# Optimization experiments

Measured on AMD Instinct MI355X. Metric: run time of the kernel, lower is better.

## Reference

```python
import jax, jax.numpy as jnp
import numpy as np

N = 50000     # nodes
E = 800000    # edges (avg degree 16)
IN = 128
HID = 128
OUT = 128


def _init_lin(key, n_out, n_in, bias=True):
    k1, k2 = jax.random.split(key)
    bound = 1.0 / np.sqrt(n_in)
    W = jax.random.uniform(k1, (n_out, n_in), minval=-bound, maxval=bound, dtype=jnp.float32)
    if bias:
        b = jax.random.uniform(k2, (n_out,), minval=-bound, maxval=bound, dtype=jnp.float32)
        return W, b
    return W


def setup_inputs() -> dict:
    key = jax.random.key(0)
    ks = jax.random.split(key, 20)
    inp = {
        "s": jax.random.normal(ks[0], (N, IN), dtype=jnp.float32),
        "t": jax.random.normal(ks[1], (N, IN), dtype=jnp.float32),
        "edge_index": jax.random.randint(ks[2], (2, E), 0, N, dtype=jnp.int64),
        "edge_weight": jax.random.normal(ks[3], (E,), dtype=jnp.float32),
    }
    dims = [(HID, IN), (OUT, HID)]
    i = 4
    for layer in range(2):
        n_out, n_in = dims[layer]
        for pre in ("s", "t"):
            Wl, bl = _init_lin(ks[i], n_out, n_in, bias=True); i += 1
            Wr = _init_lin(ks[i], n_out, n_in, bias=False); i += 1
            inp[f"{pre}{layer}_Wl"] = Wl
            inp[f"{pre}{layer}_bl"] = bl
            inp[f"{pre}{layer}_Wr"] = Wr
    return inp


def _sage(x, src, dst, w, Wl, bl, Wr):
    """SAGEConv (mean aggr, weighted messages): lin_l(mean_j w_ij x_j) + lin_r(x_i)."""
    n = x.shape[0]
    msg = x[src] * w[:, None]                                   # [E, d] gather
    agg = jax.ops.segment_sum(msg, dst, num_segments=n)         # [N, d] scatter-add
    cnt = jax.ops.segment_sum(jnp.ones_like(w), dst, num_segments=n)
    mean = agg / jnp.maximum(cnt, 1.0)[:, None]
    return mean @ Wl.T + bl + x @ Wr.T


def reference(s, t, edge_index, edge_weight,
              s0_Wl, s0_bl, s0_Wr, t0_Wl, t0_bl, t0_Wr,
              s1_Wl, s1_bl, s1_Wr, t1_Wl, t1_bl, t1_Wr):
    w = jax.nn.sigmoid(edge_weight)
    src, dst = edge_index[0], edge_index[1]
    # layer 0 (relu; dropout is identity in eval mode)
    s1 = jax.nn.relu(_sage(t, src, dst, w, s0_Wl, s0_bl, s0_Wr))
    t1 = jax.nn.relu(_sage(s, dst, src, w, t0_Wl, t0_bl, t0_Wr))  # flipped edges
    # layer 1 (no activation)
    s2 = _sage(t1, src, dst, w, s1_Wl, s1_bl, s1_Wr)
    t2 = _sage(s1, dst, src, w, t1_Wl, t1_bl, t1_Wr)
    return (s2, t2)
```

## Files before the change

kernel.cpp:

```cpp
#include <hip/hip_runtime.h>
#include <hip/hip_bf16.h>

#define DIM 128
#define BINSHIFT 8
#define BINSZ 256
#define MAXBINS2 400
#define EPB 2048
#define CAP 6144

typedef __attribute__((ext_vector_type(4))) float f32x4;
typedef __attribute__((ext_vector_type(8))) _Float16 h16x8;
typedef __attribute__((ext_vector_type(2))) _Float16 h16x2;
typedef __attribute__((ext_vector_type(8))) unsigned short u16x8;

static __device__ __forceinline__ unsigned short f2h(float f) {
    _Float16 h = (_Float16)f;
    return __builtin_bit_cast(unsigned short, h);
}

#if __has_builtin(__builtin_amdgcn_fdot2)
static __device__ __forceinline__ float dot2(h16x2 a, h16x2 b, float c) {
    return __builtin_amdgcn_fdot2(a, b, c, false);
}
#else
static __device__ __forceinline__ float dot2(h16x2 a, h16x2 b, float c) {
    return c + (float)a.x * (float)b.x + (float)a.y * (float)b.y;
}
#endif

struct WPtrs { const float* Wl[4]; const float* Wr[4]; };

__global__ __launch_bounds__(256) void dgnn_prep(
        const float* __restrict__ s, const float* __restrict__ t,
        unsigned short* __restrict__ sb, unsigned short* __restrict__ tb,
        int n4, int cvtb, WPtrs wp, unsigned short* __restrict__ Wc, int wbase,
        int* __restrict__ binCur, int nb2) {
    int b = blockIdx.x;
    if (b < wbase) {
        int which = (b >= cvtb) ? 1 : 0;
        int i = (b - which * cvtb) * 256 + threadIdx.x;
        if (i >= n4) return;
        const float* src = which ? t : s;
        unsigned short* dst = which ? tb : sb;
        float4 v = ((const float4*)src)[i];
        ushort4 o;
        o.x = f2h(v.x); o.y = f2h(v.y); o.z = f2h(v.z); o.w = f2h(v.w);
        ((ushort4*)dst)[i] = o;
    } else if (b < wbase + 128) {
        int tid = (b - wbase) * 256 + threadIdx.x;
        int i4 = tid << 2;
        int conv = i4 >> 15;
        int rem = i4 & 32767;
        int ch = rem >> 8;
        int k = rem & 255;
        const float* src = (k < 128) ? wp.Wl[conv] : wp.Wr[conv];
        float4 v = *(const float4*)(src + ch * DIM + (k & 127));
        ushort4 o;
        o.x = f2h(v.x); o.y = f2h(v.y); o.z = f2h(v.z); o.w = f2h(v.w);
        *(ushort4*)(Wc + i4) = o;
    } else {
        for (int i = threadIdx.x; i < nb2; i += 256) binCur[i] = 0;
    }
}

__global__ __launch_bounds__(256) void dgnn_binscatter(const float* __restrict__ ew,
        const int* __restrict__ srcI, const int* __restrict__ dstI,
        int* __restrict__ binCur, int2* __restrict__ binned, int E, int NBINS) {
    __shared__ int hist[MAXBINS2];
    __shared__ int epk[EPB];
    __shared__ int ewb[EPB];
    const int nb2 = 2 * NBINS;
    for (int i = threadIdx.x; i < nb2; i += 256) hist[i] = 0;
    __syncthreads();
    int base = blockIdx.x * EPB;
    int end = min(base + EPB, E);
    int cnt = end - base;
    for (int j = threadIdx.x; j < cnt; j += 256) {
        int e = base + j;
        int d = dstI[e], s = srcI[e];
        float x = ew[e];
        float w = 1.0f / (1.0f + expf(-x));
        epk[j] = d | (s << 16);
        ewb[j] = __float_as_int(w);
        atomicAdd(&hist[d >> BINSHIFT], 1);
        atomicAdd(&hist[NBINS + (s >> BINSHIFT)], 1);
    }
    __syncthreads();
    for (int i = threadIdx.x; i < nb2; i += 256) {
        int c = hist[i];
        int st = c ? atomicAdd(&binCur[i], c) : 0;
        hist[i] = i * CAP + st;
    }
    __syncthreads();
    for (int j = threadIdx.x; j < cnt; j += 256) {
        int pk = epk[j];
        int wb = ewb[j];
        int d = pk & 0xffff, s = (pk >> 16) & 0xffff;
        int pd = atomicAdd(&hist[d >> BINSHIFT], 1);
        binned[pd] = make_int2(pk, wb);
        int ps = atomicAdd(&hist[NBINS + (s >> BINSHIFT)], 1);
        binned[ps] = make_int2(pk, wb);
    }
}

__global__ __launch_bounds__(256) void dgnn_csrfinal(const int2* __restrict__ binned,
        const int* __restrict__ binCur,
        int* __restrict__ offsD, int* __restrict__ degD,
        int* __restrict__ offsS, int* __restrict__ degS,
        unsigned int* __restrict__ nbrPD, unsigned int* __restrict__ nbrPS,
        int N, int NBINS) {
    int b = blockIdx.x;
    bool isD = b < NBINS;
    int lb = isD ? b : b - NBINS;
    int nodeBase = lb << BINSHIFT;
    const int2* bin = binned + (size_t)b * CAP;
    int K = binCur[b]; if (K > CAP) K = CAP;
    int* offs = isD ? offsD : offsS;
    int* dga  = isD ? degD : degS;
    unsigned int* out = (isD ? nbrPD : nbrPS) + (size_t)lb * CAP;

    __shared__ int cnt[BINSZ], cur[BINSZ], scanb[BINSZ];
    cnt[threadIdx.x] = 0;
    __syncthreads();
    for (int i = threadIdx.x; i < K; i += 256) {
        int pk = bin[i].x;
        int node = isD ? (pk & 0xffff) : ((pk >> 16) & 0xffff);
        atomicAdd(&cnt[node - nodeBase], 1);
    }
    __syncthreads();
    int v = cnt[threadIdx.x];
    scanb[threadIdx.x] = v;
    __syncthreads();
#pragma unroll
    for (int o = 1; o < 256; o <<= 1) {
        int u = (threadIdx.x >= o) ? scanb[threadIdx.x - o] : 0;
        __syncthreads();
        scanb[threadIdx.x] += u;
        __syncthreads();
    }
    int pos = scanb[threadIdx.x] - v;
    cur[threadIdx.x] = pos;
    int n = nodeBase + threadIdx.x;
    if (n < N) { offs[n] = lb * CAP + pos; dga[n] = v; }
    __syncthreads();
    for (int i = threadIdx.x; i < K; i += 256) {
        int2 en = bin[i];
        int node, nbr;
        if (isD) { node = en.x & 0xffff; nbr = (en.x >> 16) & 0xffff; }
        else     { node = (en.x >> 16) & 0xffff; nbr = en.x & 0xffff; }
        int p = atomicAdd(&cur[node - nodeBase], 1);
        unsigned short wh = f2h(__int_as_float(en.y));
        out[p] = (unsigned int)nbr | ((unsigned int)wh << 16);
    }
}

__global__ __launch_bounds__(256, 8) void dgnn_gather2(
        const unsigned short* __restrict__ xbD, const int* __restrict__ offsD,
        const int* __restrict__ degD, const unsigned int* __restrict__ nbrD,
        unsigned short* __restrict__ meanD,
        const unsigned short* __restrict__ xbS, const int* __restrict__ offsS,
        const int* __restrict__ degS, const unsigned int* __restrict__ nbrS,
        unsigned short* __restrict__ meanS,
        int N, int halfb) {
    int which = (blockIdx.x >= halfb) ? 1 : 0;
    const unsigned short* xb = which ? xbS : xbD;
    const int* offs          = which ? offsS : offsD;
    const int* dga           = which ? degS : degD;
    const unsigned int* nbrP = which ? nbrS : nbrD;
    unsigned short* meanb    = which ? meanS : meanD;

    long long gid = (long long)(blockIdx.x - which * halfb) * 256 + threadIdx.x;
    int n = (int)(gid >> 5);
    if (n >= N) return;
    const int l32 = (int)gid & 31;
    const int q2  = l32 >> 4;
    const int m   = l32 & 15;

    int beg = offs[n];
    int dg  = dga[n];
    int end = beg + dg;
    float acc[8];
#pragma unroll
    for (int k = 0; k < 8; k++) acc[k] = 0.f;

    for (int base = beg; base < end; base += 32) {
        int cnt = end - base; if (cnt > 32) cnt = 32;
        bool inb = (base + l32) < end;
        unsigned int pk_l = inb ? nbrP[base + l32] : 0u;

        int it = 0;
        for (; it + 16 <= cnt; it += 16) {
            int e0 = it + (q2 << 1);
            unsigned int p[8];
#pragma unroll
            for (int j = 0; j < 4; j++) {
                p[2 * j]     = __shfl(pk_l, e0 + 4 * j, 32);
                p[2 * j + 1] = __shfl(pk_l, e0 + 4 * j + 1, 32);
            }
            uint4 v[8];
#pragma unroll
            for (int j = 0; j < 8; j++)
                v[j] = *(const uint4*)(xb + ((size_t)(p[j] & 0xffffu) << 7) + (m << 3));
#pragma unroll
            for (int j = 0; j < 4; j++) {
                h16x2 wp = __builtin_bit_cast(h16x2,
                    __builtin_amdgcn_perm(p[2 * j + 1], p[2 * j], 0x07060302u));
                const unsigned int* ua = &v[2 * j].x;
                const unsigned int* ub = &v[2 * j + 1].x;
#pragma unroll
                for (int k = 0; k < 4; k++) {
                    h16x2 lo = __builtin_bit_cast(h16x2,
                        __builtin_amdgcn_perm(ub[k], ua[k], 0x05040100u));
                    h16x2 hi = __builtin_bit_cast(h16x2,
                        __builtin_amdgcn_perm(ub[k], ua[k], 0x07060302u));
                    acc[2 * k]     = dot2(wp, lo, acc[2 * k]);
                    acc[2 * k + 1] = dot2(wp, hi, acc[2 * k + 1]);
                }
            }
        }
        for (; it < cnt; it += 4) {
            int e0 = it + (q2 << 1);
            unsigned int pa = __shfl(pk_l, e0, 32);
            unsigned int pb = __shfl(pk_l, e0 + 1, 32);
            uint4 va = *(const uint4*)(xb + ((size_t)(pa & 0xffffu) << 7) + (m << 3));
            uint4 vb = *(const uint4*)(xb + ((size_t)(pb & 0xffffu) << 7) + (m << 3));
            h16x2 wp = __builtin_bit_cast(h16x2,
                __builtin_amdgcn_perm(pb, pa, 0x07060302u));
            const unsigned int* ua = &va.x;
            const unsigned int* ub = &vb.x;
#pragma unroll
            for (int k = 0; k < 4; k++) {
                h16x2 lo = __builtin_bit_cast(h16x2,
                    __builtin_amdgcn_perm(ub[k], ua[k], 0x05040100u));
                h16x2 hi = __builtin_bit_cast(h16x2,
                    __builtin_amdgcn_perm(ub[k], ua[k], 0x07060302u));
                acc[2 * k]     = dot2(wp, lo, acc[2 * k]);
                acc[2 * k + 1] = dot2(wp, hi, acc[2 * k + 1]);
            }
        }
    }

#pragma unroll
    for (int k = 0; k < 8; k++)
        acc[k] += __shfl_xor(acc[k], 16);

    if (q2 == 0) {
        float inv = 1.0f / fmaxf((float)dg, 1.0f);
        u16x8 o;
#pragma unroll
        for (int k = 0; k < 8; k++) o[k] = f2h(acc[k] * inv);
        *(u16x8*)(meanb + ((size_t)n << 7) + (m << 3)) = o;
    }
}

__global__ __launch_bounds__(256) void dgnn_node2(
        const unsigned short* __restrict__ meanA, const unsigned short* __restrict__ xbA,
        const unsigned short* __restrict__ WcA, const float* __restrict__ biasA,
        float* __restrict__ outfA, unsigned short* __restrict__ outbA,
        const unsigned short* __restrict__ meanB, const unsigned short* __restrict__ xbB,
        const unsigned short* __restrict__ WcB, const float* __restrict__ biasB,
        float* __restrict__ outfB, unsigned short* __restrict__ outbB,
        int N, int mode, int halfb) {
    __shared__ __align__(16) unsigned short sW[128 * 256];

    int which = (blockIdx.x >= halfb) ? 1 : 0;
    const unsigned short* meanb = which ? meanB : meanA;
    const unsigned short* xb    = which ? xbB : xbA;
    const unsigned short* Wc    = which ? WcB : WcA;
    const float* bias           = which ? biasB : biasA;
    float* outf                 = which ? outfB : outfA;
    unsigned short* outb        = which ? outbB : outbA;
    int lb = blockIdx.x - which * halfb;

    for (int i = threadIdx.x; i < 4096; i += 256) {
        int ch = i >> 5;
        int off = (i & 31) << 4;
        float4 v = *(const float4*)((const char*)Wc + ((size_t)i << 4));
        int soff = off ^ ((ch & 7) << 4);
        *(float4*)((char*)sW + ch * 512 + soff) = v;
    }
    __syncthreads();

    const int wid = threadIdx.x >> 6;
    const int lane = threadIdx.x & 63;
    const int r = lane & 15;
    const int q = lane >> 4;
    const int ntiles = (N + 15) >> 4;

    for (int tile = lb * 4 + wid; tile < ntiles; tile += halfb * 4) {
        const int n0 = tile << 4;
        const unsigned short* A0 = meanb + (size_t)(n0 + r) * DIM + q * 8;
        const unsigned short* A1 = xb    + (size_t)(n0 + r) * DIM + q * 8;

        f32x4 acc[8];
#pragma unroll
        for (int ct = 0; ct < 8; ct++) acc[ct] = (f32x4){0.f, 0.f, 0.f, 0.f};

#pragma unroll
        for (int ks = 0; ks < 8; ks++) {
            h16x8 a = (ks < 4) ? *(const h16x8*)(A0 + ks * 32)
                               : *(const h16x8*)(A1 + (ks - 4) * 32);
#pragma unroll
            for (int ct = 0; ct < 8; ct++) {
                int ch = ct * 16 + r;
                int soff = (ks * 64 + q * 16) ^ ((ch & 7) << 4);
                h16x8 b = *(const h16x8*)((const char*)sW + ch * 512 + soff);
                acc[ct] = __builtin_amdgcn_mfma_f32_16x16x32_f16(a, b, acc[ct], 0, 0, 0);
            }
        }

#pragma unroll
        for (int ct = 0; ct < 8; ct++) {
            int ch = ct * 16 + r;
            float bv = bias[ch];
#pragma unroll
            for (int rr = 0; rr < 4; rr++) {
                int n = n0 + q * 4 + rr;
                if (n >= N) break;
                float v = acc[ct][rr] + bv;
                if (mode) {
                    v = fmaxf(v, 0.f);
                    outb[(size_t)n * DIM + ch] = f2h(v);
                } else {
                    outf[(size_t)n * DIM + ch] = v;
                }
            }
        }
    }
}

extern "C" void kernel_launch(void* const* d_in, const int* in_sizes, int n_in,
                              void* d_out, int out_size, void* d_ws, size_t ws_size,
                              hipStream_t stream) {
    const float* s  = (const float*)d_in[0];
    const float* t  = (const float*)d_in[1];
    const int*   ei = (const int*)d_in[2];
    const float* ew = (const float*)d_in[3];
    const float* s0_Wl = (const float*)d_in[4];
    const float* s0_bl = (const float*)d_in[5];
    const float* s0_Wr = (const float*)d_in[6];
    const float* t0_Wl = (const float*)d_in[7];
    const float* t0_bl = (const float*)d_in[8];
    const float* t0_Wr = (const float*)d_in[9];
    const float* s1_Wl = (const float*)d_in[10];
    const float* s1_bl = (const float*)d_in[11];
    const float* s1_Wr = (const float*)d_in[12];
    const float* t1_Wl = (const float*)d_in[13];
    const float* t1_bl = (const float*)d_in[14];
    const float* t1_Wr = (const float*)d_in[15];

    const int N = in_sizes[0] / DIM;
    const int E = in_sizes[3];
    const int NBINS = (N + BINSZ - 1) / BINSZ;

    unsigned int* nbrPD = (unsigned int*)d_ws;
    unsigned int* nbrPS = nbrPD + (size_t)NBINS * CAP;
    unsigned short* up = (unsigned short*)(nbrPS + (size_t)NBINS * CAP);
    unsigned short* sb    = up;
    unsigned short* tb    = sb    + (size_t)N * DIM;
    unsigned short* meanA = tb    + (size_t)N * DIM;
    unsigned short* meanB = meanA + (size_t)N * DIM;
    unsigned short* s1b   = meanB + (size_t)N * DIM;
    unsigned short* t1b   = s1b   + (size_t)N * DIM;
    unsigned short* Wc    = t1b   + (size_t)N * DIM;
    int* ip     = (int*)(Wc + 4 * 128 * 256);
    int* binCur = ip;
    int* offsD  = binCur + 2 * NBINS;
    int* degD   = offsD + N;
    int* offsS  = degD + N;
    int* degS   = offsS + N;

    int2* binned = (int2*)meanA;

    float* sout = (float*)d_out;
    float* tout = sout + (size_t)N * DIM;

    const int* srcI = ei;
    const int* dstI = ei + E;

    const int binb = (E + EPB - 1) / EPB;
    const int gbH = (int)(((long long)N * 32 + 255) / 256);
    const int nodeb = 256;
    const int cvtb = ((N * DIM / 4) + 255) / 256;

    WPtrs wp;
    wp.Wl[0] = s0_Wl; wp.Wr[0] = s0_Wr;
    wp.Wl[1] = t0_Wl; wp.Wr[1] = t0_Wr;
    wp.Wl[2] = s1_Wl; wp.Wr[2] = s1_Wr;
    wp.Wl[3] = t1_Wl; wp.Wr[3] = t1_Wr;
    dgnn_prep<<<2 * cvtb + 129, 256, 0, stream>>>(s, t, sb, tb, N * DIM / 4,
                                                  cvtb, wp, Wc, 2 * cvtb,
                                                  binCur, 2 * NBINS);

    dgnn_binscatter<<<binb, 256, 0, stream>>>(ew, srcI, dstI, binCur, binned, E, NBINS);
    dgnn_csrfinal<<<2 * NBINS, 256, 0, stream>>>(binned, binCur,
                                                 offsD, degD, offsS, degS,
                                                 nbrPD, nbrPS, N, NBINS);

    dgnn_gather2<<<2 * gbH, 256, 0, stream>>>(tb, offsD, degD, nbrPD, meanA,
                                              sb, offsS, degS, nbrPS, meanB, N, gbH);
    dgnn_node2<<<2 * nodeb, 256, 0, stream>>>(
        meanA, tb, Wc,         s0_bl, nullptr, s1b,
        meanB, sb, Wc + 32768, t0_bl, nullptr, t1b, N, 1, nodeb);

    dgnn_gather2<<<2 * gbH, 256, 0, stream>>>(t1b, offsD, degD, nbrPD, meanA,
                                              s1b, offsS, degS, nbrPS, meanB, N, gbH);
    dgnn_node2<<<2 * nodeb, 256, 0, stream>>>(
        meanA, t1b, Wc + 2 * 32768, s1_bl, sout, nullptr,
        meanB, s1b, Wc + 3 * 32768, t1_bl, tout, nullptr, N, 0, nodeb);
}
```

Baseline: 227.2 us.

## Split per-node gather across four wavefronts by channel slice

Replaces the half-wave-per-node gather with a layout where each node's 128 channels are split into four 32-channel slices. Each slice goes to a full 64-lane wavefront in a separate block, with direction and slice interleaved in the block index. Each lane now issues 4-byte loads over four edges per step instead of 16-byte loads, and reduces with two cross-lane xors. The aim is more waves in flight to hide gather latency, at the cost of four times more narrow load instructions and duplicated offset/degree/neighbor-list reads per node.

```diff
diff --git a/kernel.cpp b/kernel.cpp
--- a/kernel.cpp
+++ b/kernel.cpp
@@ -11,7 +11,6 @@
 typedef __attribute__((ext_vector_type(4))) float f32x4;
 typedef __attribute__((ext_vector_type(8))) _Float16 h16x8;
 typedef __attribute__((ext_vector_type(2))) _Float16 h16x2;
-typedef __attribute__((ext_vector_type(8))) unsigned short u16x8;
 
 static __device__ __forceinline__ unsigned short f2h(float f) {
     _Float16 h = (_Float16)f;
@@ -154,102 +153,72 @@
     }
 }
 
-__global__ __launch_bounds__(256, 8) void dgnn_gather2(
+__global__ __launch_bounds__(256, 8) void dgnn_gather3(
         const unsigned short* __restrict__ xbD, const int* __restrict__ offsD,
         const int* __restrict__ degD, const unsigned int* __restrict__ nbrD,
         unsigned short* __restrict__ meanD,
         const unsigned short* __restrict__ xbS, const int* __restrict__ offsS,
         const int* __restrict__ degS, const unsigned int* __restrict__ nbrS,
         unsigned short* __restrict__ meanS,
-        int N, int halfb) {
-    int which = (blockIdx.x >= halfb) ? 1 : 0;
-    const unsigned short* xb = which ? xbS : xbD;
-    const int* offs          = which ? offsS : offsD;
-    const int* dga           = which ? degS : degD;
-    const unsigned int* nbrP = which ? nbrS : nbrD;
-    unsigned short* meanb    = which ? meanS : meanD;
-
-    long long gid = (long long)(blockIdx.x - which * halfb) * 256 + threadIdx.x;
-    int n = (int)(gid >> 5);
+        int N) {
+    const int sel = blockIdx.x & 7;
+    const int dir = sel >> 2;
+    const int j   = sel & 3;
+    const unsigned short* xb = dir ? xbS : xbD;
+    const int* offs          = dir ? offsS : offsD;
+    const int* dga           = dir ? degS : degD;
+    const unsigned int* nbrP = dir ? nbrS : nbrD;
+    unsigned short* meanb    = dir ? meanS : meanD;
+
+    const int wid  = threadIdx.x >> 6;
+    const int lane = threadIdx.x & 63;
+    const int n = (blockIdx.x >> 3) * 4 + wid;
     if (n >= N) return;
-    const int l32 = (int)gid & 31;
-    const int q2  = l32 >> 4;
-    const int m   = l32 & 15;
-
-    int beg = offs[n];
-    int dg  = dga[n];
-    int end = beg + dg;
-    float acc[8];
-#pragma unroll
-    for (int k = 0; k < 8; k++) acc[k] = 0.f;
-
-    for (int base = beg; base < end; base += 32) {
-        int cnt = end - base; if (cnt > 32) cnt = 32;
-        bool inb = (base + l32) < end;
-        unsigned int pk_l = inb ? nbrP[base + l32] : 0u;
-
-        int it = 0;
-        for (; it + 16 <= cnt; it += 16) {
-            int e0 = it + (q2 << 1);
-            unsigned int p[8];
-#pragma unroll
-            for (int j = 0; j < 4; j++) {
-                p[2 * j]     = __shfl(pk_l, e0 + 4 * j, 32);
-                p[2 * j + 1] = __shfl(pk_l, e0 + 4 * j + 1, 32);
-            }
-            uint4 v[8];
-#pragma unroll
-            for (int j = 0; j < 8; j++)
-                v[j] = *(const uint4*)(xb + ((size_t)(p[j] & 0xffffu) << 7) + (m << 3));
-#pragma unroll
-            for (int j = 0; j < 4; j++) {
-                h16x2 wp = __builtin_bit_cast(h16x2,
-                    __builtin_amdgcn_perm(p[2 * j + 1], p[2 * j], 0x07060302u));
-                const unsigned int* ua = &v[2 * j].x;
-                const unsigned int* ub = &v[2 * j + 1].x;
-#pragma unroll
-                for (int k = 0; k < 4; k++) {
-                    h16x2 lo = __builtin_bit_cast(h16x2,
-                        __builtin_amdgcn_perm(ub[k], ua[k], 0x05040100u));
-                    h16x2 hi = __builtin_bit_cast(h16x2,
-                        __builtin_amdgcn_perm(ub[k], ua[k], 0x07060302u));
-                    acc[2 * k]     = dot2(wp, lo, acc[2 * k]);
-                    acc[2 * k + 1] = dot2(wp, hi, acc[2 * k + 1]);
-                }
-            }
+    const int g4 = lane >> 4;
+    const int c  = lane & 15;
+
+    const int beg = offs[n];
+    const int dg  = dga[n];
+    const int end = beg + dg;
+    const size_t chOff = (size_t)(j << 5) + (c << 1);
+
+    float a0 = 0.f, a1 = 0.f;
+
+    for (int base = beg; base < end; base += 64) {
+        int cnt = end - base; if (cnt > 64) cnt = 64;
+        unsigned int pk_l = (base + lane < end) ? nbrP[base + lane] : 0u;
+
+        for (int it = 0; it < cnt; it += 16) {
+            int e0 = it + (g4 << 1);
+            unsigned int pa = __shfl(pk_l, e0, 64);
+            unsigned int pb = __shfl(pk_l, e0 + 1, 64);
+            unsigned int pc = __shfl(pk_l, e0 + 8, 64);
+            unsigned int pd = __shfl(pk_l, e0 + 9, 64);
+            unsigned int va = *(const unsigned int*)(xb + ((size_t)(pa & 0xffffu) << 7) + chOff);
+            unsigned int vb = *(const unsigned int*)(xb + ((size_t)(pb & 0xffffu) << 7) + chOff);
+            unsigned int vc = *(const unsigned int*)(xb + ((size_t)(pc & 0xffffu) << 7) + chOff);
+            unsigned int vd = *(const unsigned int*)(xb + ((size_t)(pd & 0xffffu) << 7) + chOff);
+            h16x2 wp0 = __builtin_bit_cast(h16x2, __builtin_amdgcn_perm(pb, pa, 0x07060302u));
+            h16x2 wp1 = __builtin_bit_cast(h16x2, __builtin_amdgcn_perm(pd, pc, 0x07060302u));
+            h16x2 lo0 = __builtin_bit_cast(h16x2, __builtin_amdgcn_perm(vb, va, 0x05040100u));
+            h16x2 hi0 = __builtin_bit_cast(h16x2, __builtin_amdgcn_perm(vb, va, 0x07060302u));
+            h16x2 lo1 = __builtin_bit_cast(h16x2, __builtin_amdgcn_perm(vd, vc, 0x05040100u));
+            h16x2 hi1 = __builtin_bit_cast(h16x2, __builtin_amdgcn_perm(vd, vc, 0x07060302u));
+            a0 = dot2(wp0, lo0, a0);
+            a1 = dot2(wp0, hi0, a1);
+            a0 = dot2(wp1, lo1, a0);
+            a1 = dot2(wp1, hi1, a1);
         }
-        for (; it < cnt; it += 4) {
-            int e0 = it + (q2 << 1);
-            unsigned int pa = __shfl(pk_l, e0, 32);
-            unsigned int pb = __shfl(pk_l, e0 + 1, 32);
-            uint4 va = *(const uint4*)(xb + ((size_t)(pa & 0xffffu) << 7) + (m << 3));
-            uint4 vb = *(const uint4*)(xb + ((size_t)(pb & 0xffffu) << 7) + (m << 3));
-            h16x2 wp = __builtin_bit_cast(h16x2,
-                __builtin_amdgcn_perm(pb, pa, 0x07060302u));
-            const unsigned int* ua = &va.x;
-            const unsigned int* ub = &vb.x;
-#pragma unroll
-            for (int k = 0; k < 4; k++) {
-                h16x2 lo = __builtin_bit_cast(h16x2,
-                    __builtin_amdgcn_perm(ub[k], ua[k], 0x05040100u));
-                h16x2 hi = __builtin_bit_cast(h16x2,
-                    __builtin_amdgcn_perm(ub[k], ua[k], 0x07060302u));
-                acc[2 * k]     = dot2(wp, lo, acc[2 * k]);
-                acc[2 * k + 1] = dot2(wp, hi, acc[2 * k + 1]);
-            }
-        }
-    }
-
-#pragma unroll
-    for (int k = 0; k < 8; k++)
-        acc[k] += __shfl_xor(acc[k], 16);
-
-    if (q2 == 0) {
+    }
+
+    a0 += __shfl_xor(a0, 16); a0 += __shfl_xor(a0, 32);
+    a1 += __shfl_xor(a1, 16); a1 += __shfl_xor(a1, 32);
+
+    if (lane < 16) {
         float inv = 1.0f / fmaxf((float)dg, 1.0f);
-        u16x8 o;
-#pragma unroll
-        for (int k = 0; k < 8; k++) o[k] = f2h(acc[k] * inv);
-        *(u16x8*)(meanb + ((size_t)n << 7) + (m << 3)) = o;
+        unsigned int o = (unsigned int)f2h(a0 * inv)
+                       | ((unsigned int)f2h(a1 * inv) << 16);
+        *(unsigned int*)(meanb + ((size_t)n << 7) + chOff) = o;
     }
 }
 
@@ -379,7 +348,7 @@
     const int* dstI = ei + E;
 
     const int binb = (E + EPB - 1) / EPB;
-    const int gbH = (int)(((long long)N * 32 + 255) / 256);
+    const int g3 = ((N + 3) >> 2) << 3;
     const int nodeb = 256;
     const int cvtb = ((N * DIM / 4) + 255) / 256;
 
@@ -397,14 +366,14 @@
                                                  offsD, degD, offsS, degS,
                                                  nbrPD, nbrPS, N, NBINS);
 
-    dgnn_gather2<<<2 * gbH, 256, 0, stream>>>(tb, offsD, degD, nbrPD, meanA,
-                                              sb, offsS, degS, nbrPS, meanB, N, gbH);
+    dgnn_gather3<<<g3, 256, 0, stream>>>(tb, offsD, degD, nbrPD, meanA,
+                                         sb, offsS, degS, nbrPS, meanB, N);
     dgnn_node2<<<2 * nodeb, 256, 0, stream>>>(
         meanA, tb, Wc,         s0_bl, nullptr, s1b,
         meanB, sb, Wc + 32768, t0_bl, nullptr, t1b, N, 1, nodeb);
 
-    dgnn_gather2<<<2 * gbH, 256, 0, stream>>>(t1b, offsD, degD, nbrPD, meanA,
-                                              s1b, offsS, degS, nbrPS, meanB, N, gbH);
+    dgnn_gather3<<<g3, 256, 0, stream>>>(t1b, offsD, degD, nbrPD, meanA,
+                                         s1b, offsS, degS, nbrPS, meanB, N);
     dgnn_node2<<<2 * nodeb, 256, 0, stream>>>(
         meanA, t1b, Wc + 2 * 32768, s1_bl, sout, nullptr,
         meanB, s1b, Wc + 3 * 32768, t1_bl, tout, nullptr, N, 0, nodeb);
```

Measured after the change: 365.2 us. +60.7%, slower.
